# Kernel tuning notes

Hardware: AMD Instinct MI355X
Metric: run time of the kernel (lower is better)

The kernel has to match this reference:

```python
import jax, jax.numpy as jnp
import numpy as np
import math

B, S, DIM = 2, 2048, 1024
H, KVH = 16, 4
HD = DIM // H          # 64, head dim
WINDOW = 256           # sliding-window size (0 = global)
ROPE_BASE = 10000.0
EPS = 1e-6


def setup_inputs() -> dict:
    key = jax.random.key(0)
    ks = jax.random.split(key, 6)
    s = 0.02
    return {
        "x": jax.random.normal(ks[0], (B, S, DIM), jnp.float32),
        "Wq": jax.random.normal(ks[1], (DIM, DIM), jnp.float32) * s,
        "Wk": jax.random.normal(ks[2], (KVH * HD, DIM), jnp.float32) * s,
        "Wv": jax.random.normal(ks[3], (KVH * HD, DIM), jnp.float32) * s,
        "Wo": jax.random.normal(ks[4], (DIM, DIM), jnp.float32) * s,
        "q_gain": jnp.ones((H,), jnp.float32),
        "pair_mix": jnp.tile(jnp.eye(2, dtype=jnp.float32), (H // 2, 1, 1))
                    + 0.01 * jax.random.normal(ks[5], (H // 2, 2, 2), jnp.float32),
    }


def _rms_norm(v):
    # F.rms_norm over last dim, no learned weight
    return v * jax.lax.rsqrt(jnp.mean(v * v, axis=-1, keepdims=True) + EPS)


def _rope_tables(seqlen, dtype):
    inv_freq = 1.0 / (ROPE_BASE ** (jnp.arange(0, HD, 2, dtype=jnp.float32) / HD))  # [HD/2]
    t = jnp.arange(seqlen, dtype=jnp.float32)
    freqs = jnp.outer(t, inv_freq)                        # [S, HD/2]
    return jnp.cos(freqs).astype(dtype)[None, None], jnp.sin(freqs).astype(dtype)[None, None]


def _apply_rotary(v, cos, sin):
    half = v.shape[-1] // 2
    v1, v2 = v[..., :half], v[..., half:]
    return jnp.concatenate((v1 * cos + v2 * sin, -v1 * sin + v2 * cos), axis=-1)


def reference(x, Wq, Wk, Wv, Wo, q_gain, pair_mix):
    bsz, seqlen, dim = x.shape
    q = (x @ Wq.T).reshape(bsz, seqlen, H, HD).transpose(0, 2, 1, 3)    # [B,H,S,D]
    k = (x @ Wk.T).reshape(bsz, seqlen, KVH, HD).transpose(0, 2, 1, 3)  # [B,KV,S,D]
    v = (x @ Wv.T).reshape(bsz, seqlen, KVH, HD).transpose(0, 2, 1, 3)

    q = _rms_norm(q)
    k = _rms_norm(k)
    cos, sin = _rope_tables(seqlen, q.dtype)
    q = _apply_rotary(q, cos, sin)
    k = _apply_rotary(k, cos, sin)
    q = q * q_gain.astype(q.dtype)[None, :, None, None]

    # GQA expansion (repeat_interleave over head axis)
    rep = H // KVH
    k_full = jnp.repeat(k, rep, axis=1)  # [B,H,S,D]
    v_full = jnp.repeat(v, rep, axis=1)

    # sliding-window causal mask: attend iff 0 <= i-j < WINDOW
    pos = jnp.arange(seqlen)
    mask = (pos[:, None] >= pos[None, :]) & (pos[:, None] - pos[None, :] < WINDOW)

    scale = 1.0 / math.sqrt(HD)
    scores = jnp.einsum('bhqd,bhkd->bhqk', q, k_full) * scale
    scores = jnp.where(mask[None, None], scores, jnp.finfo(scores.dtype).min)
    att = jax.nn.softmax(scores, axis=-1)
    y = jnp.einsum('bhqk,bhkd->bhqd', att, v_full)  # [B,H,S,D]

    # paired-head mixing: mix each consecutive head pair with a 2x2 matrix
    yp = y.reshape(bsz, H // 2, 2, seqlen, HD)
    y = jnp.einsum('bpitd,poi->bpotd', yp, pair_mix.astype(y.dtype)).reshape(bsz, H, seqlen, HD)

    out = y.transpose(0, 2, 1, 3).reshape(bsz, seqlen, dim) @ Wo.T
    return out
```

## Files before the change

kernel.cpp:

```cpp
#include <hip/hip_runtime.h>
#include <hip/hip_bf16.h>
#include <cstdint>

#define S_LEN 2048
#define QKV_COLS 1536

typedef __bf16 bf16_t;
typedef bf16_t bf16x8 __attribute__((ext_vector_type(8)));
typedef bf16_t bf16x4 __attribute__((ext_vector_type(4)));
typedef float f32x4 __attribute__((ext_vector_type(4)));

typedef __attribute__((address_space(1))) void as1_void;
typedef __attribute__((address_space(3))) void as3_void;

__device__ __forceinline__ void async_load16(const void* g, void* lds) {
  __builtin_amdgcn_global_load_lds(
      (as1_void*)(uintptr_t)g,
      (as3_void*)(uint32_t)(uintptr_t)lds,
      16, 0, 0);
}

__device__ __forceinline__ uint32_t pkbf(float a, float b) {
  union { bf16_t h[2]; uint32_t u; } c;
  c.h[0] = (bf16_t)a; c.h[1] = (bf16_t)b;
  return c.u;
}

__global__ __launch_bounds__(256) void convert_all(
    const float4* __restrict__ x, const float4* __restrict__ wq,
    const float4* __restrict__ wk, const float4* __restrict__ wv,
    const float4* __restrict__ wo, const float* __restrict__ pm,
    bf16x4* __restrict__ xb, bf16x4* __restrict__ wqkvb, bf16x4* __restrict__ wob) {
  int u = blockIdx.x * 256 + threadIdx.x;
  if (u >= 1441792) {
    int off = u - 1441792;
    int flat = off * 4;
    int row = flat >> 10, colf = flat & 1023;
    int col2p = colf & ~64;
    int p = colf >> 7, ii = (colf >> 6) & 1;
    float4 a = wo[(row * 1024 + col2p) >> 2];
    float4 bq = wo[(row * 1024 + (col2p | 64)) >> 2];
    float m0v = pm[p * 4 + ii], m1v = pm[p * 4 + 2 + ii];
    bf16x4 o4;
    o4[0] = (bf16_t)(m0v * a.x + m1v * bq.x);
    o4[1] = (bf16_t)(m0v * a.y + m1v * bq.y);
    o4[2] = (bf16_t)(m0v * a.z + m1v * bq.z);
    o4[3] = (bf16_t)(m0v * a.w + m1v * bq.w);
    wob[off] = o4;
    return;
  }
  const float4* src; bf16x4* dst; int off;
  if (u < 1048576)      { src = x;  dst = xb;             off = u; }
  else if (u < 1310720) { src = wq; dst = wqkvb;          off = u - 1048576; }
  else if (u < 1376256) { src = wk; dst = wqkvb + 262144; off = u - 1310720; }
  else                  { src = wv; dst = wqkvb + 327680; off = u - 1376256; }
  float4 f = src[off];
  bf16x4 o;
  o[0] = (bf16_t)f.x; o[1] = (bf16_t)f.y; o[2] = (bf16_t)f.z; o[3] = (bf16_t)f.w;
  dst[off] = o;
}

__global__ __launch_bounds__(256) void gemm_qkv(
    const bf16_t* __restrict__ A, const bf16_t* __restrict__ B,
    bf16_t* __restrict__ C, bf16_t* __restrict__ vt,
    const float* __restrict__ q_gain, int N, int K) {
  __shared__ bf16_t As[2][64 * 64];
  __shared__ bf16_t Bs[2][128 * 64];
  const int tid = threadIdx.x;
  const int lane = tid & 63;
  const int w = tid >> 6;
  const int wm = (w & 1) << 5, wn = (w >> 1) << 6;
  const int orig = blockIdx.y * gridDim.x + blockIdx.x;
  const int id = (orig & 7) * 96 + (orig >> 3);
  const int m0 = (id / 12) << 6, n0 = (id % 12) << 7;
  const int fidx = lane & 15, quad = lane >> 4;
  f32x4 acc[2][4] = {};
  int ra0 = (tid + 0) >> 3,   sa0 = ((tid + 0) & 7) ^ (ra0 & 7);
  int ra1 = (tid + 256) >> 3, sa1 = ((tid + 256) & 7) ^ (ra1 & 7);
  const bf16_t* Ag0 = A + (size_t)(m0 + ra0) * K + sa0 * 8;
  const bf16_t* Ag1 = A + (size_t)(m0 + ra1) * K + sa1 * 8;
  const bf16_t* Bg[4];
#pragma unroll
  for (int j = 0; j < 4; j++) {
    int c = tid + j * 256, r = c >> 3, s = (c & 7) ^ (r & 7);
    Bg[j] = B + (size_t)(n0 + r) * K + s * 8;
  }
  int aoff[2][2], boff[4][2];
#pragma unroll
  for (int mi = 0; mi < 2; mi++) {
    int row = wm + mi * 16 + fidx;
#pragma unroll
    for (int half = 0; half < 2; half++)
      aoff[mi][half] = row * 64 + (((half * 4 + quad) ^ (row & 7)) * 8);
  }
#pragma unroll
  for (int ni = 0; ni < 4; ni++) {
    int row = wn + ni * 16 + fidx;
#pragma unroll
    for (int half = 0; half < 2; half++)
      boff[ni][half] = row * 64 + (((half * 4 + quad) ^ (row & 7)) * 8);
  }
  async_load16(Ag0, &As[0][tid * 8]);
  async_load16(Ag1, &As[0][(tid + 256) * 8]);
#pragma unroll
  for (int j = 0; j < 4; j++)
    async_load16(Bg[j], &Bs[0][(tid + j * 256) * 8]);
  int cur = 0;
  for (int kt = 0; kt < K; kt += 64) {
    const int nk = kt + 64;
    if (nk < K) {
      async_load16(Ag0 + nk, &As[cur ^ 1][tid * 8]);
      async_load16(Ag1 + nk, &As[cur ^ 1][(tid + 256) * 8]);
#pragma unroll
      for (int j = 0; j < 4; j++)
        async_load16(Bg[j] + nk, &Bs[cur ^ 1][(tid + j * 256) * 8]);
      asm volatile("s_waitcnt vmcnt(6)" ::: "memory");
    } else {
      asm volatile("s_waitcnt vmcnt(0)" ::: "memory");
    }
    __builtin_amdgcn_s_barrier();
    __builtin_amdgcn_sched_barrier(0);
    bf16x8 af[2][2], bfr[4][2];
#pragma unroll
    for (int mi = 0; mi < 2; mi++)
#pragma unroll
      for (int half = 0; half < 2; half++)
        af[mi][half] = *(const bf16x8*)(&As[cur][aoff[mi][half]]);
#pragma unroll
    for (int ni = 0; ni < 4; ni++)
#pragma unroll
      for (int half = 0; half < 2; half++)
        bfr[ni][half] = *(const bf16x8*)(&Bs[cur][boff[ni][half]]);
#pragma unroll
    for (int half = 0; half < 2; half++)
#pragma unroll
      for (int mi = 0; mi < 2; mi++)
#pragma unroll
        for (int ni = 0; ni < 4; ni++)
          acc[mi][ni] = __builtin_amdgcn_mfma_f32_16x16x32_bf16(
              af[mi][half], bfr[ni][half], acc[mi][ni], 0, 0, 0);
    asm volatile("s_waitcnt lgkmcnt(0)" ::: "memory");
    __builtin_amdgcn_s_barrier();
    cur ^= 1;
  }
  const int hc0 = n0 + wn;
  if (hc0 >= 1280) {
#pragma unroll
    for (int mi = 0; mi < 2; mi++)
#pragma unroll
      for (int ni = 0; ni < 4; ni++) {
        int cg = (hc0 - 1280) + ni * 16 + fidx;
        int g = cg >> 6, dh = cg & 63;
        int srow = m0 + wm + mi * 16 + quad * 4;
        int bb = srow >> 11, si = srow & (S_LEN - 1);
        bf16x4 pack;
#pragma unroll
        for (int r = 0; r < 4; r++) pack[r] = (bf16_t)acc[mi][ni][r];
        *(bf16x4*)(vt + ((size_t)((bb * 4 + g) * 64 + dh)) * S_LEN + si) = pack;
      }
    return;
  }
  float gain = 1.f;
  if (hc0 < 1024) gain = q_gain[hc0 >> 6] * 0.125f;
#pragma unroll
  for (int mi = 0; mi < 2; mi++)
#pragma unroll
    for (int r = 0; r < 4; r++) {
      float ss = 0.f;
#pragma unroll
      for (int ni = 0; ni < 4; ni++) { float t = acc[mi][ni][r]; ss += t * t; }
#pragma unroll
      for (int off = 8; off >= 1; off >>= 1) ss += __shfl_xor(ss, off);
      float scl = rsqrtf(ss * (1.f / 64.f) + 1e-6f);
      int s = (m0 + wm + mi * 16 + quad * 4 + r) & (S_LEN - 1);
#pragma unroll
      for (int ni = 0; ni < 2; ni++) {
        float v1 = acc[mi][ni][r] * scl;
        float v2 = acc[mi][ni + 2][r] * scl;
        float fr = (float)(ni * 16 + fidx);
        float ang = (float)s * __expf(fr * -0.28782313662425575f);
        float sn, cs;
        __sincosf(ang, &sn, &cs);
        acc[mi][ni][r]     = (v1 * cs + v2 * sn) * gain;
        acc[mi][ni + 2][r] = (-v1 * sn + v2 * cs) * gain;
      }
    }
#pragma unroll
  for (int mi = 0; mi < 2; mi++)
#pragma unroll
    for (int ni = 0; ni < 4; ni++)
#pragma unroll
      for (int r = 0; r < 4; r++) {
        int gr = m0 + wm + mi * 16 + quad * 4 + r;
        int gc = n0 + wn + ni * 16 + fidx;
        C[(size_t)gr * N + gc] = (bf16_t)acc[mi][ni][r];
      }
}

__global__ __launch_bounds__(256) void gemm_bt_f32(
    const bf16_t* __restrict__ A, const bf16_t* __restrict__ B,
    float* __restrict__ C, int N, int K) {
  __shared__ bf16_t As[2][64 * 64];
  __shared__ bf16_t Bs[2][128 * 64];
  const int tid = threadIdx.x;
  const int lane = tid & 63;
  const int w = tid >> 6;
  const int wm = (w & 1) << 5, wn = (w >> 1) << 6;
  const int orig = blockIdx.y * gridDim.x + blockIdx.x;
  const int id = (orig & 7) * 64 + (orig >> 3);
  const int m0 = (id >> 3) << 6, n0 = (id & 7) << 7;
  const int fidx = lane & 15, quad = lane >> 4;
  f32x4 acc[2][4] = {};
  int ra0 = (tid + 0) >> 3,   sa0 = ((tid + 0) & 7) ^ (ra0 & 7);
  int ra1 = (tid + 256) >> 3, sa1 = ((tid + 256) & 7) ^ (ra1 & 7);
  const bf16_t* Ag0 = A + (size_t)(m0 + ra0) * K + sa0 * 8;
  const bf16_t* Ag1 = A + (size_t)(m0 + ra1) * K + sa1 * 8;
  const bf16_t* Bg[4];
#pragma unroll
  for (int j = 0; j < 4; j++) {
    int c = tid + j * 256, r = c >> 3, s = (c & 7) ^ (r & 7);
    Bg[j] = B + (size_t)(n0 + r) * K + s * 8;
  }
  int aoff[2][2], boff[4][2];
#pragma unroll
  for (int mi = 0; mi < 2; mi++) {
    int row = wm + mi * 16 + fidx;
#pragma unroll
    for (int half = 0; half < 2; half++)
      aoff[mi][half] = row * 64 + (((half * 4 + quad) ^ (row & 7)) * 8);
  }
#pragma unroll
  for (int ni = 0; ni < 4; ni++) {
    int row = wn + ni * 16 + fidx;
#pragma unroll
    for (int half = 0; half < 2; half++)
      boff[ni][half] = row * 64 + (((half * 4 + quad) ^ (row & 7)) * 8);
  }
  async_load16(Ag0, &As[0][tid * 8]);
  async_load16(Ag1, &As[0][(tid + 256) * 8]);
#pragma unroll
  for (int j = 0; j < 4; j++)
    async_load16(Bg[j], &Bs[0][(tid + j * 256) * 8]);
  int cur = 0;
  for (int kt = 0; kt < K; kt += 64) {
    const int nk = kt + 64;
    if (nk < K) {
      async_load16(Ag0 + nk, &As[cur ^ 1][tid * 8]);
      async_load16(Ag1 + nk, &As[cur ^ 1][(tid + 256) * 8]);
#pragma unroll
      for (int j = 0; j < 4; j++)
        async_load16(Bg[j] + nk, &Bs[cur ^ 1][(tid + j * 256) * 8]);
      asm volatile("s_waitcnt vmcnt(6)" ::: "memory");
    } else {
      asm volatile("s_waitcnt vmcnt(0)" ::: "memory");
    }
    __builtin_amdgcn_s_barrier();
    __builtin_amdgcn_sched_barrier(0);
    bf16x8 af[2][2], bfr[4][2];
#pragma unroll
    for (int mi = 0; mi < 2; mi++)
#pragma unroll
      for (int half = 0; half < 2; half++)
        af[mi][half] = *(const bf16x8*)(&As[cur][aoff[mi][half]]);
#pragma unroll
    for (int ni = 0; ni < 4; ni++)
#pragma unroll
      for (int half = 0; half < 2; half++)
        bfr[ni][half] = *(const bf16x8*)(&Bs[cur][boff[ni][half]]);
#pragma unroll
    for (int half = 0; half < 2; half++)
#pragma unroll
      for (int mi = 0; mi < 2; mi++)
#pragma unroll
        for (int ni = 0; ni < 4; ni++)
          acc[mi][ni] = __builtin_amdgcn_mfma_f32_16x16x32_bf16(
              af[mi][half], bfr[ni][half], acc[mi][ni], 0, 0, 0);
    asm volatile("s_waitcnt lgkmcnt(0)" ::: "memory");
    __builtin_amdgcn_s_barrier();
    cur ^= 1;
  }
#pragma unroll
  for (int mi = 0; mi < 2; mi++)
#pragma unroll
    for (int ni = 0; ni < 4; ni++)
#pragma unroll
      for (int r = 0; r < 4; r++) {
        int gr = m0 + wm + mi * 16 + quad * 4 + r;
        int gc = n0 + wn + ni * 16 + fidx;
        C[(size_t)gr * N + gc] = acc[mi][ni][r];
      }
}

#define FIXMAX 8.0f
#define OST 72
__global__ __launch_bounds__(256) void attn_mfma(
    const bf16_t* __restrict__ qkv, const bf16_t* __restrict__ vt,
    bf16_t* __restrict__ yb) {
  __shared__ bf16_t ob[4][32 * OST];
  const int tid = threadIdx.x, lane = tid & 63, w = tid >> 6;
  const int col = lane & 15, quad = lane >> 4;
  const int orig = blockIdx.z * 256 + blockIdx.y * 64 + blockIdx.x;
  const int id = (orig & 7) * 64 + (orig >> 3);
  const int q0 = (id & 63) * 32, g = (id >> 6) & 3, b = id >> 8;
  const int h = g * 4 + w;

  bf16x8 qf[2][2];
#pragma unroll
  for (int t = 0; t < 2; t++) {
    const bf16_t* qb =
        qkv + ((size_t)b * S_LEN + q0 + t * 16 + col) * QKV_COLS + h * 64 + quad * 8;
    qf[t][0] = *(const bf16x8*)qb;
    qf[t][1] = *(const bf16x8*)(qb + 32);
  }
  const bf16_t* kbase = qkv + (size_t)b * S_LEN * QKV_COLS + 1024 + g * 64 + quad * 8;
  const bf16_t* vbase = vt + ((size_t)((b * 4 + g) * 64) + col) * S_LEN + quad * 8;

  f32x4 o[2][4] = {};
  float ps[2] = {};

  const int c_lo = max(0, (q0 - 255) >> 5);
  const int c_hi = (q0 + 31) >> 5;
  for (int c = c_lo; c <= c_hi; c++) {
    const int k0 = c * 32;
    bf16x8 kf[2][2];
#pragma unroll
    for (int nt = 0; nt < 2; nt++) {
      const bf16_t* kp = kbase + (size_t)(k0 + nt * 16 + col) * QKV_COLS;
      kf[nt][0] = *(const bf16x8*)kp;
      kf[nt][1] = *(const bf16x8*)(kp + 32);
    }
    bf16x8 vf[4];
#pragma unroll
    for (int nt2 = 0; nt2 < 4; nt2++)
      vf[nt2] = *(const bf16x8*)(vbase + (size_t)(nt2 * 16) * S_LEN + k0);

#pragma unroll
    for (int t = 0; t < 2; t++) {
      const int qt0 = q0 + t * 16;
      if (k0 > qt0 + 15) continue;
      f32x4 st[2];
#pragma unroll
      for (int nt = 0; nt < 2; nt++) {
        f32x4 a = {};
        a = __builtin_amdgcn_mfma_f32_16x16x32_bf16(kf[nt][0], qf[t][0], a, 0, 0, 0);
        a = __builtin_amdgcn_mfma_f32_16x16x32_bf16(kf[nt][1], qf[t][1], a, 0, 0, 0);
        st[nt] = a;
      }
      const bool needmask = (k0 + 31 > qt0) || (k0 < qt0 - 224);
      float p2[2][4];
      if (needmask) {
        int q = qt0 + col;
#pragma unroll
        for (int nt = 0; nt < 2; nt++)
#pragma unroll
          for (int r = 0; r < 4; r++) {
            int k = k0 + nt * 16 + quad * 4 + r;
            bool valid = (k <= q) && (q - k < 256);
            p2[nt][r] = valid ? __expf(st[nt][r] - FIXMAX) : 0.f;
          }
      } else {
#pragma unroll
        for (int nt = 0; nt < 2; nt++)
#pragma unroll
          for (int r = 0; r < 4; r++)
            p2[nt][r] = __expf(st[nt][r] - FIXMAX);
      }
#pragma unroll
      for (int nt = 0; nt < 2; nt++)
#pragma unroll
        for (int r = 0; r < 4; r++) ps[t] += p2[nt][r];
      uint32_t pk0[2], pk1[2];
      pk0[0] = pkbf(p2[0][0], p2[0][1]); pk0[1] = pkbf(p2[0][2], p2[0][3]);
      pk1[0] = pkbf(p2[1][0], p2[1][1]); pk1[1] = pkbf(p2[1][2], p2[1][3]);
      uint32_t w32[4];
#pragma unroll
      for (int m = 0; m < 4; m++) {
        int srclane = col + 16 * ((2 * quad + (m >> 1)) & 3);
        uint32_t a0 = (uint32_t)__shfl((int)pk0[m & 1], srclane);
        uint32_t a1 = (uint32_t)__shfl((int)pk1[m & 1], srclane);
        w32[m] = (quad < 2) ? a0 : a1;
      }
      union { uint32_t u[4]; bf16x8 v; } pu;
      pu.u[0] = w32[0]; pu.u[1] = w32[1]; pu.u[2] = w32[2]; pu.u[3] = w32[3];
      bf16x8 pf = pu.v;
#pragma unroll
      for (int nt2 = 0; nt2 < 4; nt2++)
        o[t][nt2] = __builtin_amdgcn_mfma_f32_16x16x32_bf16(pf, vf[nt2], o[t][nt2], 0, 0, 0);
    }
  }
#pragma unroll
  for (int t = 0; t < 2; t++) {
    float v = ps[t];
    v += __shfl_xor(v, 16);
    v += __shfl_xor(v, 32);
    float il = 1.f / v;
    float il4[4];
#pragma unroll
    for (int r = 0; r < 4; r++) il4[r] = __shfl(il, quad * 4 + r);
    int row0 = t * 16 + quad * 4;
#pragma unroll
    for (int nt2 = 0; nt2 < 4; nt2++)
#pragma unroll
      for (int r = 0; r < 4; r++)
        ob[w][(row0 + r) * OST + nt2 * 16 + col] = (bf16_t)(o[t][nt2][r] * il4[r]);
  }
  asm volatile("s_waitcnt lgkmcnt(0)" ::: "memory");
#pragma unroll
  for (int it = 0; it < 4; it++) {
    int row = it * 8 + (lane >> 3);
    int d0 = (lane & 7) * 8;
    bf16x8 v8 = *(const bf16x8*)(ob[w] + row * OST + d0);
    *(bf16x8*)(yb + ((size_t)b * S_LEN + q0 + row) * 1024 + h * 64 + d0) = v8;
  }
}

extern "C" void kernel_launch(void* const* d_in, const int* in_sizes, int n_in,
                              void* d_out, int out_size, void* d_ws, size_t ws_size,
                              hipStream_t stream) {
  const float* x        = (const float*)d_in[0];
  const float* Wq       = (const float*)d_in[1];
  const float* Wk       = (const float*)d_in[2];
  const float* Wv       = (const float*)d_in[3];
  const float* Wo       = (const float*)d_in[4];
  const float* q_gain   = (const float*)d_in[5];
  const float* pair_mix = (const float*)d_in[6];
  float* out = (float*)d_out;

  bf16_t* ws    = (bf16_t*)d_ws;
  bf16_t* xb    = ws;
  bf16_t* wqkvb = xb + 4096 * 1024;
  bf16_t* wob   = wqkvb + 1536 * 1024;
  bf16_t* qkvb  = wob + 1024 * 1024;
  bf16_t* yb    = qkvb + 4096 * 1536;
  bf16_t* vt    = yb + 4096 * 1024;

  convert_all<<<6656, 256, 0, stream>>>(
      (const float4*)x, (const float4*)Wq, (const float4*)Wk, (const float4*)Wv,
      (const float4*)Wo, pair_mix, (bf16x4*)xb, (bf16x4*)wqkvb, (bf16x4*)wob);
  gemm_qkv<<<dim3(12, 64), 256, 0, stream>>>(xb, wqkvb, qkvb, vt, q_gain, 1536, 1024);
  attn_mfma<<<dim3(64, 4, 2), 256, 0, stream>>>(qkvb, vt, yb);
  gemm_bt_f32<<<dim3(8, 64), 256, 0, stream>>>(yb, wob, out, 1024, 1024);
}
```

Baseline: 137.6 us.

## Split attention key range across two wave groups and merge partials in LDS

Doubles the attention block to 512 threads. Two groups of four waves each process half of the key chunks for the same heads, and the second group writes its partial outputs and row sums to shared memory for the first group to combine. Because softmax uses a fixed max (FIXMAX), the partials can be added directly. This adds parallelism to the latency-bound attention kernel, which has only 512 blocks, at the cost of extra LDS use, a block-wide barrier and higher register pressure per block.

```diff
diff --git a/kernel.cpp b/kernel.cpp
--- a/kernel.cpp
+++ b/kernel.cpp
@@ -293,16 +293,19 @@
 
 #define FIXMAX 8.0f
 #define OST 72
-__global__ __launch_bounds__(256) void attn_mfma(
+__global__ __launch_bounds__(512) void attn_mfma(
     const bf16_t* __restrict__ qkv, const bf16_t* __restrict__ vt,
     bf16_t* __restrict__ yb) {
+  __shared__ f32x4 po[4][2][4][64];
+  __shared__ float pps[4][2][64];
   __shared__ bf16_t ob[4][32 * OST];
   const int tid = threadIdx.x, lane = tid & 63, w = tid >> 6;
+  const int hw = w & 3, sp = w >> 2;
   const int col = lane & 15, quad = lane >> 4;
   const int orig = blockIdx.z * 256 + blockIdx.y * 64 + blockIdx.x;
   const int id = (orig & 7) * 64 + (orig >> 3);
   const int q0 = (id & 63) * 32, g = (id >> 6) & 3, b = id >> 8;
-  const int h = g * 4 + w;
+  const int h = g * 4 + hw;
 
   bf16x8 qf[2][2];
 #pragma unroll
@@ -320,7 +323,12 @@
 
   const int c_lo = max(0, (q0 - 255) >> 5);
   const int c_hi = (q0 + 31) >> 5;
-  for (int c = c_lo; c <= c_hi; c++) {
+  const int nc = c_hi - c_lo + 1;
+  const int c_mid = c_lo + ((nc + 1) >> 1);
+  const int my_lo = sp ? c_mid : c_lo;
+  const int my_hi = sp ? c_hi : (c_mid - 1);
+
+  for (int c = my_lo; c <= my_hi; c++) {
     const int k0 = c * 32;
     bf16x8 kf[2][2];
 #pragma unroll
@@ -388,29 +396,46 @@
         o[t][nt2] = __builtin_amdgcn_mfma_f32_16x16x32_bf16(pf, vf[nt2], o[t][nt2], 0, 0, 0);
     }
   }
-#pragma unroll
-  for (int t = 0; t < 2; t++) {
-    float v = ps[t];
-    v += __shfl_xor(v, 16);
-    v += __shfl_xor(v, 32);
-    float il = 1.f / v;
-    float il4[4];
-#pragma unroll
-    for (int r = 0; r < 4; r++) il4[r] = __shfl(il, quad * 4 + r);
-    int row0 = t * 16 + quad * 4;
-#pragma unroll
-    for (int nt2 = 0; nt2 < 4; nt2++)
-#pragma unroll
-      for (int r = 0; r < 4; r++)
-        ob[w][(row0 + r) * OST + nt2 * 16 + col] = (bf16_t)(o[t][nt2][r] * il4[r]);
-  }
-  asm volatile("s_waitcnt lgkmcnt(0)" ::: "memory");
-#pragma unroll
-  for (int it = 0; it < 4; it++) {
-    int row = it * 8 + (lane >> 3);
-    int d0 = (lane & 7) * 8;
-    bf16x8 v8 = *(const bf16x8*)(ob[w] + row * OST + d0);
-    *(bf16x8*)(yb + ((size_t)b * S_LEN + q0 + row) * 1024 + h * 64 + d0) = v8;
+  if (sp) {
+#pragma unroll
+    for (int t = 0; t < 2; t++) {
+#pragma unroll
+      for (int nt2 = 0; nt2 < 4; nt2++) po[hw][t][nt2][lane] = o[t][nt2];
+      pps[hw][t][lane] = ps[t];
+    }
+  }
+  __syncthreads();
+  if (sp == 0) {
+#pragma unroll
+    for (int t = 0; t < 2; t++) {
+#pragma unroll
+      for (int nt2 = 0; nt2 < 4; nt2++) o[t][nt2] += po[hw][t][nt2][lane];
+      ps[t] += pps[hw][t][lane];
+    }
+#pragma unroll
+    for (int t = 0; t < 2; t++) {
+      float v = ps[t];
+      v += __shfl_xor(v, 16);
+      v += __shfl_xor(v, 32);
+      float il = 1.f / v;
+      float il4[4];
+#pragma unroll
+      for (int r = 0; r < 4; r++) il4[r] = __shfl(il, quad * 4 + r);
+      int row0 = t * 16 + quad * 4;
+#pragma unroll
+      for (int nt2 = 0; nt2 < 4; nt2++)
+#pragma unroll
+        for (int r = 0; r < 4; r++)
+          ob[hw][(row0 + r) * OST + nt2 * 16 + col] = (bf16_t)(o[t][nt2][r] * il4[r]);
+    }
+    asm volatile("s_waitcnt lgkmcnt(0)" ::: "memory");
+#pragma unroll
+    for (int it = 0; it < 4; it++) {
+      int row = it * 8 + (lane >> 3);
+      int d0 = (lane & 7) * 8;
+      bf16x8 v8 = *(const bf16x8*)(ob[hw] + row * OST + d0);
+      *(bf16x8*)(yb + ((size_t)b * S_LEN + q0 + row) * 1024 + h * 64 + d0) = v8;
+    }
   }
 }
 
@@ -438,6 +463,6 @@
       (const float4*)x, (const float4*)Wq, (const float4*)Wk, (const float4*)Wv,
       (const float4*)Wo, pair_mix, (bf16x4*)xb, (bf16x4*)wqkvb, (bf16x4*)wob);
   gemm_qkv<<<dim3(12, 64), 256, 0, stream>>>(xb, wqkvb, qkvb, vt, q_gain, 1536, 1024);
-  attn_mfma<<<dim3(64, 4, 2), 256, 0, stream>>>(qkvb, vt, yb);
+  attn_mfma<<<dim3(64, 4, 2), 512, 0, stream>>>(qkvb, vt, yb);
   gemm_bt_f32<<<dim3(8, 64), 256, 0, stream>>>(yb, wob, out, 1024, 1024);
 }
```

Result: no change. 138.0 us, median of 2 (+0.3%).
